# Kernel tuning notes

Measured on AMD Instinct MI355X. Metric: run time of the kernel, lower is better.

## Reference

```python
import jax, jax.numpy as jnp
import numpy as np

N, E = 50000, 800000
IN, HID, OUT = 256, 128, 128


def setup_inputs() -> dict:
    key = jax.random.key(0)
    ks = jax.random.split(key, 6)
    x = jax.random.normal(ks[0], (N, IN), dtype=jnp.float32)
    edge_index = jax.random.randint(ks[1], (2, E), 0, N, dtype=jnp.int32)
    # xavier_normal-ish scales (exact init values irrelevant for correctness baseline)
    W1 = jax.random.normal(ks[2], (IN, HID), dtype=jnp.float32) * (1.414 / np.sqrt(IN))
    att_src = jax.random.normal(ks[3], (HID,), dtype=jnp.float32) * 0.1
    att_dst = jax.random.normal(ks[4], (HID,), dtype=jnp.float32) * 0.1
    W2 = jax.random.normal(ks[5], (HID, OUT), dtype=jnp.float32) * (1.414 / np.sqrt(HID))
    return {"x": x, "edge_index": edge_index, "W1": W1,
            "att_src": att_src, "att_dst": att_dst, "W2": W2}


def _gat_layer(x, edge_index, W, a_src, a_dst):
    """GATConv(heads=1, concat=False, add_self_loops=False, dropout=0), attention=True."""
    n = x.shape[0]
    src, dst = edge_index[0], edge_index[1]  # message x_j = h[src], grouped by index = dst
    h = x @ W                                 # (N, C)
    e_src = h @ a_src                         # (N,) per-node attention logits
    e_dst = h @ a_dst                         # (N,)
    # per-edge: sigmoid(alpha_j + alpha_i), then scatter-softmax over dst neighborhoods
    alpha = jax.nn.sigmoid(e_src[src] + e_dst[dst])             # (E,)
    m = jax.ops.segment_max(alpha, dst, num_segments=n)          # stable softmax max
    ex = jnp.exp(alpha - m[dst])
    denom = jax.ops.segment_sum(ex, dst, num_segments=n)
    w = ex / denom[dst]                                          # (E,)
    # scatter-add aggregation of weighted source features; heads=1 so mean over heads is identity
    return jax.ops.segment_sum(h[src] * w[:, None], dst, num_segments=n)  # (N, C)


def reference(x, edge_index, W1, att_src, att_dst, W2):
    h1 = jax.nn.elu(_gat_layer(x, edge_index, W1, att_src, att_dst))
    # conv2 called with attention=False: mm(h1, W2).view(N,1,C).mean(1) == plain linear
    return h1 @ W2
```

## Files before the change

### kernel.cpp

```cpp
#include <hip/hip_runtime.h>
#include <hip/hip_bf16.h>

#define N_NODES 50000
#define N_EDGES 800000
#define DIN 256
#define DHID 128
#define DOUT 128
#define NBUCK 196
#define BINBLK 256
#define EPB 3125
#define G1TILES 391
#define HTP 136

typedef __attribute__((ext_vector_type(8))) short bf16x8;
typedef __attribute__((ext_vector_type(4))) float f32x4;

__device__ inline unsigned short f2b(float f) {
    __hip_bfloat16 b = __float2bfloat16(f);
    return *reinterpret_cast<unsigned short*>(&b);
}

__global__ __launch_bounds__(1024) void convW_lhist_kernel(
    const float* __restrict__ W1, const float* __restrict__ W2,
    const int* __restrict__ ei,
    unsigned short* __restrict__ W1t, unsigned short* __restrict__ W2t,
    int* __restrict__ blockHistT)
{
    __shared__ int h[NBUCK];
    const int blk = blockIdx.x;
    const int tid = threadIdx.x;

    if (blk < 48) {
        int i = blk * 1024 + tid;
        if (i < DIN * DHID) {
            int n = i >> 8, k = i & 255;
            int kt = k >> 5, q = (k >> 3) & 3, e = k & 7;
            int t = n >> 4, m = n & 15;
            W1t[(((kt * 8 + t) * 64) + (q * 16 + m)) * 8 + e] = f2b(W1[k * DHID + n]);
        } else {
            int j = i - DIN * DHID;
            int n = j >> 7, k = j & 127;
            int kt = k >> 5, q = (k >> 3) & 3, e = k & 7;
            int t = n >> 4, m = n & 15;
            W2t[(((kt * 8 + t) * 64) + (q * 16 + m)) * 8 + e] = f2b(W2[k * DOUT + n]);
        }
        return;
    }

    const int b = blk - 48;
    if (tid < NBUCK) h[tid] = 0;
    __syncthreads();
    const int base = b * EPB;
    #pragma unroll 1
    for (int it = 0; it < 4; ++it) {
        int e = base + it * 1024 + tid;
        if (e < base + EPB)
            atomicAdd(&h[ei[N_EDGES + e] >> 8], 1);
    }
    __syncthreads();
    if (tid < 256) blockHistT[b * 256 + tid] = (tid < NBUCK) ? h[tid] : 0;
}

__global__ __launch_bounds__(256) void gemm1_scan_kernel(
    const float* __restrict__ x,
    const unsigned short* __restrict__ W1t,
    const float* __restrict__ att_src,
    const float* __restrict__ att_dst,
    const int* __restrict__ blockHistT,
    unsigned short* __restrict__ hb,
    float* __restrict__ es,
    float* __restrict__ ed,
    int* __restrict__ matrixScan)
{
    __shared__ int bs[256];
    __shared__ int sc[256];
    const int tid = threadIdx.x;

    if (blockIdx.x >= G1TILES) {
        const int b = blockIdx.x - G1TILES;

        int tot = 0;
        #pragma unroll 4
        for (int p = 0; p < 256; ++p) tot += blockHistT[p * 256 + tid];
        bs[tid] = tot;
        __syncthreads();
        #pragma unroll
        for (int off = 1; off < 256; off <<= 1) {
            int u = (tid >= off) ? bs[tid - off] : 0;
            __syncthreads();
            bs[tid] += u;
            __syncthreads();
        }
        const int base = (b == 0) ? 0 : bs[b - 1];

        int c = blockHistT[tid * 256 + b];
        sc[tid] = c;
        __syncthreads();
        #pragma unroll
        for (int off = 1; off < 256; off <<= 1) {
            int u = (tid >= off) ? sc[tid - off] : 0;
            __syncthreads();
            sc[tid] += u;
            __syncthreads();
        }
        matrixScan[b * 256 + tid] = base + sc[tid] - c;
        return;
    }

    const int wave = tid >> 6, lane = tid & 63;
    const int row0 = blockIdx.x * 128 + wave * 32;
    const int m = lane & 15, q = lane >> 4;

    int r0 = row0 + m;
    int r1 = row0 + 16 + m;
    int rc0 = (r0 < N_NODES) ? r0 : 0;
    int rc1 = (r1 < N_NODES) ? r1 : 0;

    f32x4 acc0[8], acc1[8];
    #pragma unroll
    for (int t = 0; t < 8; ++t) {
        acc0[t] = (f32x4){0.f, 0.f, 0.f, 0.f};
        acc1[t] = (f32x4){0.f, 0.f, 0.f, 0.f};
    }

    const float* xr0 = x + (size_t)rc0 * DIN + q * 8;
    const float* xr1 = x + (size_t)rc1 * DIN + q * 8;
    const short* wb  = (const short*)W1t + lane * 8;

    #pragma unroll
    for (int kt = 0; kt < 8; ++kt) {
        float4 f0 = *(const float4*)(xr0 + kt * 32);
        float4 f1 = *(const float4*)(xr0 + kt * 32 + 4);
        float4 g0 = *(const float4*)(xr1 + kt * 32);
        float4 g1 = *(const float4*)(xr1 + kt * 32 + 4);
        bf16x8 a0, a1;
        a0[0] = (short)f2b(f0.x); a0[1] = (short)f2b(f0.y);
        a0[2] = (short)f2b(f0.z); a0[3] = (short)f2b(f0.w);
        a0[4] = (short)f2b(f1.x); a0[5] = (short)f2b(f1.y);
        a0[6] = (short)f2b(f1.z); a0[7] = (short)f2b(f1.w);
        a1[0] = (short)f2b(g0.x); a1[1] = (short)f2b(g0.y);
        a1[2] = (short)f2b(g0.z); a1[3] = (short)f2b(g0.w);
        a1[4] = (short)f2b(g1.x); a1[5] = (short)f2b(g1.y);
        a1[6] = (short)f2b(g1.z); a1[7] = (short)f2b(g1.w);
        #pragma unroll
        for (int t = 0; t < 8; ++t) {
            bf16x8 b = *(const bf16x8*)(wb + (kt * 8 + t) * 512);
            acc0[t] = __builtin_amdgcn_mfma_f32_16x16x32_bf16(a0, b, acc0[t], 0, 0, 0);
            acc1[t] = __builtin_amdgcn_mfma_f32_16x16x32_bf16(a1, b, acc1[t], 0, 0, 0);
        }
    }

    #pragma unroll
    for (int reg = 0; reg < 4; ++reg) {
        int ra = row0 + q * 4 + reg;
        int rb = row0 + 16 + q * 4 + reg;
        if (ra < N_NODES) {
            #pragma unroll
            for (int t = 0; t < 8; ++t)
                hb[(size_t)ra * DHID + t * 16 + m] = f2b(acc0[t][reg]);
        }
        if (rb < N_NODES) {
            #pragma unroll
            for (int t = 0; t < 8; ++t)
                hb[(size_t)rb * DHID + t * 16 + m] = f2b(acc1[t][reg]);
        }
    }

    float es0[4] = {0,0,0,0}, ed0[4] = {0,0,0,0};
    float es1[4] = {0,0,0,0}, ed1[4] = {0,0,0,0};
    #pragma unroll
    for (int t = 0; t < 8; ++t) {
        float as = att_src[t * 16 + m];
        float ad = att_dst[t * 16 + m];
        #pragma unroll
        for (int reg = 0; reg < 4; ++reg) {
            es0[reg] += acc0[t][reg] * as;
            ed0[reg] += acc0[t][reg] * ad;
            es1[reg] += acc1[t][reg] * as;
            ed1[reg] += acc1[t][reg] * ad;
        }
    }
    #pragma unroll
    for (int off = 8; off; off >>= 1)
        #pragma unroll
        for (int reg = 0; reg < 4; ++reg) {
            es0[reg] += __shfl_xor(es0[reg], off);
            ed0[reg] += __shfl_xor(ed0[reg], off);
            es1[reg] += __shfl_xor(es1[reg], off);
            ed1[reg] += __shfl_xor(ed1[reg], off);
        }
    if (m == 0) {
        #pragma unroll
        for (int reg = 0; reg < 4; ++reg) {
            int ra = row0 + q * 4 + reg;
            int rb = row0 + 16 + q * 4 + reg;
            if (ra < N_NODES) { es[ra] = es0[reg]; ed[ra] = ed0[reg]; }
            if (rb < N_NODES) { es[rb] = es1[reg]; ed[rb] = ed1[reg]; }
        }
    }
}

__global__ __launch_bounds__(1024) void binpass_kernel(
    const int* __restrict__ ei,
    const float* __restrict__ es,
    const float* __restrict__ ed,
    const int* __restrict__ matrixScan,
    int2* __restrict__ binned)
{
    __shared__ int lcur[NBUCK];
    const int t = threadIdx.x, blk = blockIdx.x;
    if (t < NBUCK) lcur[t] = matrixScan[t * 256 + blk];
    __syncthreads();
    const int base = blk * EPB;
    #pragma unroll 1
    for (int it = 0; it < 4; ++it) {
        int e = base + it * 1024 + t;
        if (e < base + EPB) {
            int s = ei[e];
            int d = ei[N_EDGES + e];
            float a  = es[s] + ed[d];
            float sg = 1.f / (1.f + __expf(-a));
            float w  = __expf(sg);
            int pos = atomicAdd(&lcur[d >> 8], 1);
            binned[pos] = make_int2(s | ((d & 255) << 16), __float_as_int(w));
        }
    }
}

__global__ __launch_bounds__(1024) void sortpass_kernel(
    const int2* __restrict__ binned,
    const int* __restrict__ matrixScan,
    int2* __restrict__ sortedSW,
    int* __restrict__ offset,
    int* __restrict__ count)
{
    __shared__ int lhist[256], lscan[256], lcur[256];
    const int t = threadIdx.x, b = blockIdx.x;
    const int start = matrixScan[b * 256];
    const int end   = (b == NBUCK - 1) ? N_EDGES : matrixScan[(b + 1) * 256];
    const int cnt   = end - start;

    if (t < 256) lhist[t] = 0;
    __syncthreads();
    for (int i = t; i < cnt; i += 1024)
        atomicAdd(&lhist[(binned[start + i].x >> 16) & 255], 1);
    __syncthreads();

    int v = 0;
    if (t < 256) { v = lhist[t]; lscan[t] = v; }
    __syncthreads();
    #pragma unroll
    for (int off = 1; off < 256; off <<= 1) {
        int u = 0;
        if (t < 256 && t >= off) u = lscan[t - off];
        __syncthreads();
        if (t < 256) lscan[t] += u;
        __syncthreads();
    }
    if (t < 256) {
        int excl = lscan[t] - v;
        int node = (b << 8) + t;
        if (node < N_NODES) { offset[node] = start + excl; count[node] = v; }
        lcur[t] = excl;
    }
    __syncthreads();

    for (int i = t; i < cnt; i += 1024) {
        int2 ent = binned[start + i];
        int dlow = (ent.x >> 16) & 255;
        int pos = atomicAdd(&lcur[dlow], 1);
        sortedSW[start + pos] = make_int2(ent.x & 0xFFFF, ent.y);
    }
}

__global__ __launch_bounds__(256) void aggemm2_kernel(
    const int2* __restrict__ sortedSW,
    const int* __restrict__ offset,
    const int* __restrict__ count,
    const unsigned short* __restrict__ hb,
    const unsigned short* __restrict__ W2t,
    float* __restrict__ out)
{
    __shared__ unsigned short ht[16][HTP];
    const int tid = threadIdx.x;
    const int wv = tid >> 6, lane = tid & 63;
    const int nbase = blockIdx.x * 16;

    #pragma unroll 1
    for (int s = 0; s < 4; ++s) {
        const int row = wv * 4 + s;
        const int node = nbase + row;

        int beg = offset[node];
        int deg = count[node];

        float2 acc = make_float2(0.f, 0.f);
        float wsum = 0.f;

        for (int bb = 0; bb < deg; bb += 64) {
            int cnt = min(64, deg - bb);
            int2 sw = (lane < cnt) ? sortedSW[beg + bb + lane] : make_int2(0, 0);
            int j = 0;

#define TIER(T)                                                                 \
            for (; j + T <= cnt; j += T) {                                      \
                unsigned uu[T]; float ww[T];                                    \
                _Pragma("unroll")                                               \
                for (int k = 0; k < T; ++k) {                                   \
                    int s_ = __builtin_amdgcn_readlane(sw.x, j + k);            \
                    uu[k] = *(const unsigned*)(hb + (size_t)s_ * DHID + 2 * lane);\
                }                                                               \
                _Pragma("unroll")                                               \
                for (int k = 0; k < T; ++k)                                     \
                    ww[k] = __uint_as_float(                                    \
                        (unsigned)__builtin_amdgcn_readlane(sw.y, j + k));      \
                _Pragma("unroll")                                               \
                for (int k = 0; k < T; ++k) {                                   \
                    wsum  += ww[k];                                             \
                    acc.x += ww[k] * __uint_as_float(uu[k] << 16);              \
                    acc.y += ww[k] * __uint_as_float(uu[k] & 0xffff0000u);      \
                }                                                               \
            }

            TIER(16)
            TIER(8)
            TIER(4)
#undef TIER
            for (; j < cnt; ++j) {
                int   sj = __builtin_amdgcn_readlane(sw.x, j);
                float wj = __uint_as_float((unsigned)__builtin_amdgcn_readlane(sw.y, j));
                unsigned u = *(const unsigned*)(hb + (size_t)sj * DHID + 2 * lane);
                acc.x += wj * __uint_as_float(u << 16);
                acc.y += wj * __uint_as_float(u & 0xffff0000u);
                wsum  += wj;
            }
        }
        float inv = (deg > 0) ? 1.f / wsum : 0.f;
        float v0 = acc.x * inv, v1 = acc.y * inv;
        float e0 = v0 > 0.f ? v0 : (__expf(v0) - 1.f);
        float e1 = v1 > 0.f ? v1 : (__expf(v1) - 1.f);
        *(unsigned*)&ht[row][2 * lane] =
            (unsigned)f2b(e0) | ((unsigned)f2b(e1) << 16);
    }
    __syncthreads();

    const int m = lane & 15, q = lane >> 4;

    f32x4 c0 = (f32x4){0.f, 0.f, 0.f, 0.f};
    f32x4 c1 = (f32x4){0.f, 0.f, 0.f, 0.f};

    const short* wb = (const short*)W2t + lane * 8;
    const int t0 = wv * 2, t1 = wv * 2 + 1;

    #pragma unroll
    for (int kt = 0; kt < 4; ++kt) {
        bf16x8 a = *(const bf16x8*)&ht[m][q * 8 + kt * 32];
        bf16x8 b0 = *(const bf16x8*)(wb + (kt * 8 + t0) * 512);
        bf16x8 b1 = *(const bf16x8*)(wb + (kt * 8 + t1) * 512);
        c0 = __builtin_amdgcn_mfma_f32_16x16x32_bf16(a, b0, c0, 0, 0, 0);
        c1 = __builtin_amdgcn_mfma_f32_16x16x32_bf16(a, b1, c1, 0, 0, 0);
    }

    #pragma unroll
    for (int reg = 0; reg < 4; ++reg) {
        int node = nbase + q * 4 + reg;
        out[(size_t)node * DOUT + t0 * 16 + m] = c0[reg];
        out[(size_t)node * DOUT + t1 * 16 + m] = c1[reg];
    }
}

extern "C" void kernel_launch(void* const* d_in, const int* in_sizes, int n_in,
                              void* d_out, int out_size, void* d_ws, size_t ws_size,
                              hipStream_t stream)
{
    const float* x    = (const float*)d_in[0];
    const int*   ei   = (const int*)d_in[1];
    const float* W1   = (const float*)d_in[2];
    const float* asrc = (const float*)d_in[3];
    const float* adst = (const float*)d_in[4];
    const float* W2   = (const float*)d_in[5];
    float*       out  = (float*)d_out;

    char* p = (char*)d_ws;
    unsigned short* hb  = (unsigned short*)p;  p += (size_t)N_NODES * DHID * 2;
    unsigned short* W1t = (unsigned short*)p;  p += (size_t)DHID * DIN * 2;
    unsigned short* W2t = (unsigned short*)p;  p += (size_t)DOUT * DHID * 2;
    float* es     = (float*)p;  p += (size_t)N_NODES * 4;
    float* ed     = (float*)p;  p += (size_t)N_NODES * 4;
    int*   offset = (int*)p;    p += (size_t)N_NODES * 4;
    int*   count  = (int*)p;    p += (size_t)N_NODES * 4;
    int*   blockHistT   = (int*)p; p += (size_t)256 * 256 * 4;
    int*   matrixScan   = (int*)p; p += (size_t)NBUCK * 256 * 4;
    int2*  binned   = (int2*)p; p += (size_t)N_EDGES * 8;
    int2*  sortedSW = (int2*)p; p += (size_t)N_EDGES * 8;

    convW_lhist_kernel<<<48 + BINBLK, 1024, 0, stream>>>(W1, W2, ei, W1t, W2t, blockHistT);

    gemm1_scan_kernel<<<G1TILES + NBUCK, 256, 0, stream>>>(
        x, W1t, asrc, adst, blockHistT, hb, es, ed, matrixScan);

    binpass_kernel<<<BINBLK, 1024, 0, stream>>>(ei, es, ed, matrixScan, binned);

    sortpass_kernel<<<NBUCK, 1024, 0, stream>>>(binned, matrixScan, sortedSW, offset, count);

    aggemm2_kernel<<<(N_NODES + 15) / 16, 256, 0, stream>>>(
        sortedSW, offset, count, hb, W2t, out);
}
```

Measured before the change: 183.9 us.

## Gather four edges per wave with 16-byte loads in aggregation kernel

```diff
diff --git a/kernel.cpp b/kernel.cpp
--- a/kernel.cpp
+++ b/kernel.cpp
@@ -286,6 +286,10 @@
     const int wv = tid >> 6, lane = tid & 63;
     const int nbase = blockIdx.x * 16;
 
+    const int  qlane = lane & 15;
+    const bool q1 = (lane >> 4) & 1;
+    const bool q2 = (lane >> 5) & 1;
+
     #pragma unroll 1
     for (int s = 0; s < 4; ++s) {
         const int row = wv * 4 + s;
@@ -294,7 +298,8 @@
         int beg = offset[node];
         int deg = count[node];
 
-        float2 acc = make_float2(0.f, 0.f);
+        float a0 = 0.f, a1 = 0.f, a2 = 0.f, a3 = 0.f;
+        float a4 = 0.f, a5 = 0.f, a6 = 0.f, a7 = 0.f;
         float wsum = 0.f;
 
         for (int bb = 0; bb < deg; bb += 64) {
@@ -302,45 +307,108 @@
             int2 sw = (lane < cnt) ? sortedSW[beg + bb + lane] : make_int2(0, 0);
             int j = 0;
 
-#define TIER(T)                                                                 \
-            for (; j + T <= cnt; j += T) {                                      \
-                unsigned uu[T]; float ww[T];                                    \
-                _Pragma("unroll")                                               \
-                for (int k = 0; k < T; ++k) {                                   \
-                    int s_ = __builtin_amdgcn_readlane(sw.x, j + k);            \
-                    uu[k] = *(const unsigned*)(hb + (size_t)s_ * DHID + 2 * lane);\
-                }                                                               \
-                _Pragma("unroll")                                               \
-                for (int k = 0; k < T; ++k)                                     \
-                    ww[k] = __uint_as_float(                                    \
-                        (unsigned)__builtin_amdgcn_readlane(sw.y, j + k));      \
-                _Pragma("unroll")                                               \
-                for (int k = 0; k < T; ++k) {                                   \
-                    wsum  += ww[k];                                             \
-                    acc.x += ww[k] * __uint_as_float(uu[k] << 16);              \
-                    acc.y += ww[k] * __uint_as_float(uu[k] & 0xffff0000u);      \
-                }                                                               \
+#define QTIER(T)                                                                 \
+            for (; j + 4 * T <= cnt; j += 4 * T) {                               \
+                uint4 uu[T]; float ww[T];                                        \
+                _Pragma("unroll")                                                \
+                for (int k = 0; k < T; ++k) {                                    \
+                    int s0 = __builtin_amdgcn_readlane(sw.x, j + 4 * k);         \
+                    int s1 = __builtin_amdgcn_readlane(sw.x, j + 4 * k + 1);     \
+                    int s2 = __builtin_amdgcn_readlane(sw.x, j + 4 * k + 2);     \
+                    int s3 = __builtin_amdgcn_readlane(sw.x, j + 4 * k + 3);     \
+                    int sl = q1 ? s1 : s0;                                       \
+                    int sh = q1 ? s3 : s2;                                       \
+                    int ss = q2 ? sh : sl;                                       \
+                    uu[k] = *(const uint4*)(hb + (size_t)ss * DHID + 8 * qlane); \
+                }                                                                \
+                _Pragma("unroll")                                                \
+                for (int k = 0; k < T; ++k) {                                    \
+                    unsigned w0 = (unsigned)__builtin_amdgcn_readlane(sw.y, j + 4 * k);     \
+                    unsigned w1 = (unsigned)__builtin_amdgcn_readlane(sw.y, j + 4 * k + 1); \
+                    unsigned w2 = (unsigned)__builtin_amdgcn_readlane(sw.y, j + 4 * k + 2); \
+                    unsigned w3 = (unsigned)__builtin_amdgcn_readlane(sw.y, j + 4 * k + 3); \
+                    unsigned wl = q1 ? w1 : w0;                                  \
+                    unsigned wh = q1 ? w3 : w2;                                  \
+                    ww[k] = __uint_as_float(q2 ? wh : wl);                       \
+                }                                                                \
+                _Pragma("unroll")                                                \
+                for (int k = 0; k < T; ++k) {                                    \
+                    float w = ww[k];                                             \
+                    wsum += w;                                                   \
+                    a0 += w * __uint_as_float(uu[k].x << 16);                    \
+                    a1 += w * __uint_as_float(uu[k].x & 0xffff0000u);            \
+                    a2 += w * __uint_as_float(uu[k].y << 16);                    \
+                    a3 += w * __uint_as_float(uu[k].y & 0xffff0000u);            \
+                    a4 += w * __uint_as_float(uu[k].z << 16);                    \
+                    a5 += w * __uint_as_float(uu[k].z & 0xffff0000u);            \
+                    a6 += w * __uint_as_float(uu[k].w << 16);                    \
+                    a7 += w * __uint_as_float(uu[k].w & 0xffff0000u);            \
+                }                                                                \
             }
 
-            TIER(16)
-            TIER(8)
-            TIER(4)
-#undef TIER
-            for (; j < cnt; ++j) {
-                int   sj = __builtin_amdgcn_readlane(sw.x, j);
-                float wj = __uint_as_float((unsigned)__builtin_amdgcn_readlane(sw.y, j));
-                unsigned u = *(const unsigned*)(hb + (size_t)sj * DHID + 2 * lane);
-                acc.x += wj * __uint_as_float(u << 16);
-                acc.y += wj * __uint_as_float(u & 0xffff0000u);
-                wsum  += wj;
+            QTIER(8)
+            QTIER(4)
+            QTIER(2)
+            QTIER(1)
+#undef QTIER
+            if (j < cnt) {
+                int last = cnt - 1;
+                int r = cnt - j;
+                int s0 = __builtin_amdgcn_readlane(sw.x, j);
+                int s1 = __builtin_amdgcn_readlane(sw.x, min(j + 1, last));
+                int s2 = __builtin_amdgcn_readlane(sw.x, min(j + 2, last));
+                int sl = q1 ? s1 : s0;
+                int sh = q1 ? s2 : s2;
+                int ss = q2 ? sh : sl;
+                uint4 u = *(const uint4*)(hb + (size_t)ss * DHID + 8 * qlane);
+                unsigned w0 = (unsigned)__builtin_amdgcn_readlane(sw.y, j);
+                unsigned w1 = (unsigned)__builtin_amdgcn_readlane(sw.y, min(j + 1, last));
+                unsigned w2 = (unsigned)__builtin_amdgcn_readlane(sw.y, min(j + 2, last));
+                int qq = (lane >> 4);
+                unsigned wl = q1 ? w1 : w0;
+                unsigned wh = w2;
+                float w = (qq < r) ? __uint_as_float(q2 ? wh : wl) : 0.f;
+                wsum += w;
+                a0 += w * __uint_as_float(u.x << 16);
+                a1 += w * __uint_as_float(u.x & 0xffff0000u);
+                a2 += w * __uint_as_float(u.y << 16);
+                a3 += w * __uint_as_float(u.y & 0xffff0000u);
+                a4 += w * __uint_as_float(u.z << 16);
+                a5 += w * __uint_as_float(u.z & 0xffff0000u);
+                a6 += w * __uint_as_float(u.w << 16);
+                a7 += w * __uint_as_float(u.w & 0xffff0000u);
             }
         }
+
+        a0 += __shfl_xor(a0, 16); a0 += __shfl_xor(a0, 32);
+        a1 += __shfl_xor(a1, 16); a1 += __shfl_xor(a1, 32);
+        a2 += __shfl_xor(a2, 16); a2 += __shfl_xor(a2, 32);
+        a3 += __shfl_xor(a3, 16); a3 += __shfl_xor(a3, 32);
+        a4 += __shfl_xor(a4, 16); a4 += __shfl_xor(a4, 32);
+        a5 += __shfl_xor(a5, 16); a5 += __shfl_xor(a5, 32);
+        a6 += __shfl_xor(a6, 16); a6 += __shfl_xor(a6, 32);
+        a7 += __shfl_xor(a7, 16); a7 += __shfl_xor(a7, 32);
+        wsum += __shfl_xor(wsum, 16); wsum += __shfl_xor(wsum, 32);
+
         float inv = (deg > 0) ? 1.f / wsum : 0.f;
-        float v0 = acc.x * inv, v1 = acc.y * inv;
+        float v0 = a0 * inv, v1 = a1 * inv, v2 = a2 * inv, v3 = a3 * inv;
+        float v4 = a4 * inv, v5 = a5 * inv, v6 = a6 * inv, v7 = a7 * inv;
         float e0 = v0 > 0.f ? v0 : (__expf(v0) - 1.f);
         float e1 = v1 > 0.f ? v1 : (__expf(v1) - 1.f);
-        *(unsigned*)&ht[row][2 * lane] =
-            (unsigned)f2b(e0) | ((unsigned)f2b(e1) << 16);
+        float e2 = v2 > 0.f ? v2 : (__expf(v2) - 1.f);
+        float e3 = v3 > 0.f ? v3 : (__expf(v3) - 1.f);
+        float e4 = v4 > 0.f ? v4 : (__expf(v4) - 1.f);
+        float e5 = v5 > 0.f ? v5 : (__expf(v5) - 1.f);
+        float e6 = v6 > 0.f ? v6 : (__expf(v6) - 1.f);
+        float e7 = v7 > 0.f ? v7 : (__expf(v7) - 1.f);
+        if (lane < 16) {
+            uint4 pk;
+            pk.x = (unsigned)f2b(e0) | ((unsigned)f2b(e1) << 16);
+            pk.y = (unsigned)f2b(e2) | ((unsigned)f2b(e3) << 16);
+            pk.z = (unsigned)f2b(e4) | ((unsigned)f2b(e5) << 16);
+            pk.w = (unsigned)f2b(e6) | ((unsigned)f2b(e7) << 16);
+            *(uint4*)&ht[row][8 * lane] = pk;
+        }
     }
     __syncthreads();
 
```

Result: slower. 190.6 us (+3.7%).

## Fuse per-bucket sort with aggregation and second GEMM using shared-memory edge buffer

Applied to the files above, without the earlier changes.

```diff
diff --git a/kernel.cpp b/kernel.cpp
--- a/kernel.cpp
+++ b/kernel.cpp
@@ -11,6 +11,7 @@
 #define EPB 3125
 #define G1TILES 391
 #define HTP 136
+#define EBCAP 8192
 
 typedef __attribute__((ext_vector_type(8))) short bf16x8;
 typedef __attribute__((ext_vector_type(4))) float f32x4;
@@ -227,145 +228,142 @@
     }
 }
 
-__global__ __launch_bounds__(1024) void sortpass_kernel(
+__global__ __launch_bounds__(1024) void sortaggemm_kernel(
     const int2* __restrict__ binned,
     const int* __restrict__ matrixScan,
-    int2* __restrict__ sortedSW,
-    int* __restrict__ offset,
-    int* __restrict__ count)
-{
-    __shared__ int lhist[256], lscan[256], lcur[256];
-    const int t = threadIdx.x, b = blockIdx.x;
-    const int start = matrixScan[b * 256];
-    const int end   = (b == NBUCK - 1) ? N_EDGES : matrixScan[(b + 1) * 256];
-    const int cnt   = end - start;
-
-    if (t < 256) lhist[t] = 0;
-    __syncthreads();
-    for (int i = t; i < cnt; i += 1024)
-        atomicAdd(&lhist[(binned[start + i].x >> 16) & 255], 1);
-    __syncthreads();
-
-    int v = 0;
-    if (t < 256) { v = lhist[t]; lscan[t] = v; }
-    __syncthreads();
-    #pragma unroll
-    for (int off = 1; off < 256; off <<= 1) {
-        int u = 0;
-        if (t < 256 && t >= off) u = lscan[t - off];
-        __syncthreads();
-        if (t < 256) lscan[t] += u;
-        __syncthreads();
-    }
-    if (t < 256) {
-        int excl = lscan[t] - v;
-        int node = (b << 8) + t;
-        if (node < N_NODES) { offset[node] = start + excl; count[node] = v; }
-        lcur[t] = excl;
-    }
-    __syncthreads();
-
-    for (int i = t; i < cnt; i += 1024) {
-        int2 ent = binned[start + i];
-        int dlow = (ent.x >> 16) & 255;
-        int pos = atomicAdd(&lcur[dlow], 1);
-        sortedSW[start + pos] = make_int2(ent.x & 0xFFFF, ent.y);
-    }
-}
-
-__global__ __launch_bounds__(256) void aggemm2_kernel(
-    const int2* __restrict__ sortedSW,
-    const int* __restrict__ offset,
-    const int* __restrict__ count,
     const unsigned short* __restrict__ hb,
     const unsigned short* __restrict__ W2t,
     float* __restrict__ out)
 {
-    __shared__ unsigned short ht[16][HTP];
+    __shared__ int2 eb[EBCAP];
+    __shared__ int lhist[256], lscan[256], lcur[256];
+    __shared__ unsigned short ht[64][HTP];
     const int tid = threadIdx.x;
+    const int b = blockIdx.x;
     const int wv = tid >> 6, lane = tid & 63;
-    const int nbase = blockIdx.x * 16;
+
+    const int start = matrixScan[b * 256];
+    const int end   = (b == NBUCK - 1) ? N_EDGES : matrixScan[(b + 1) * 256];
+    const int cnt   = end - start;
+
+    if (tid < 256) lhist[tid] = 0;
+    __syncthreads();
+    for (int i = tid; i < cnt; i += 1024)
+        atomicAdd(&lhist[(binned[start + i].x >> 16) & 255], 1);
+    __syncthreads();
+
+    int v = 0;
+    if (tid < 256) { v = lhist[tid]; lscan[tid] = v; }
+    __syncthreads();
+    #pragma unroll
+    for (int off = 1; off < 256; off <<= 1) {
+        int u = 0;
+        if (tid < 256 && tid >= off) u = lscan[tid - off];
+        __syncthreads();
+        if (tid < 256) lscan[tid] += u;
+        __syncthreads();
+    }
+    if (tid < 256) lcur[tid] = lscan[tid] - v;
+    __syncthreads();
+
+    for (int i = tid; i < cnt; i += 1024) {
+        int2 ent = binned[start + i];
+        int dlow = (ent.x >> 16) & 255;
+        int pos = atomicAdd(&lcur[dlow], 1);
+        eb[pos] = make_int2(ent.x & 0xFFFF, ent.y);
+    }
+    __syncthreads();
 
     #pragma unroll 1
-    for (int s = 0; s < 4; ++s) {
-        const int row = wv * 4 + s;
-        const int node = nbase + row;
-
-        int beg = offset[node];
-        int deg = count[node];
-
-        float2 acc = make_float2(0.f, 0.f);
-        float wsum = 0.f;
-
-        for (int bb = 0; bb < deg; bb += 64) {
-            int cnt = min(64, deg - bb);
-            int2 sw = (lane < cnt) ? sortedSW[beg + bb + lane] : make_int2(0, 0);
-            int j = 0;
+    for (int r4 = 0; r4 < 4; ++r4) {
+        const int base64 = r4 * 64;
+
+        #pragma unroll 1
+        for (int s = 0; s < 4; ++s) {
+            const int row = wv * 4 + s;
+            const int dlow = base64 + row;
+            const int beg = lscan[dlow] - lhist[dlow];
+            const int deg = lhist[dlow];
+
+            float2 acc = make_float2(0.f, 0.f);
+            float wsum = 0.f;
+
+            for (int bb = 0; bb < deg; bb += 64) {
+                int c_ = min(64, deg - bb);
+                int2 sw = (lane < c_) ? eb[beg + bb + lane] : make_int2(0, 0);
+                int j = 0;
 
 #define TIER(T)                                                                 \
-            for (; j + T <= cnt; j += T) {                                      \
-                unsigned uu[T]; float ww[T];                                    \
-                _Pragma("unroll")                                               \
-                for (int k = 0; k < T; ++k) {                                   \
-                    int s_ = __builtin_amdgcn_readlane(sw.x, j + k);            \
-                    uu[k] = *(const unsigned*)(hb + (size_t)s_ * DHID + 2 * lane);\
-                }                                                               \
-                _Pragma("unroll")                                               \
-                for (int k = 0; k < T; ++k)                                     \
-                    ww[k] = __uint_as_float(                                    \
-                        (unsigned)__builtin_amdgcn_readlane(sw.y, j + k));      \
-                _Pragma("unroll")                                               \
-                for (int k = 0; k < T; ++k) {                                   \
-                    wsum  += ww[k];                                             \
-                    acc.x += ww[k] * __uint_as_float(uu[k] << 16);              \
-                    acc.y += ww[k] * __uint_as_float(uu[k] & 0xffff0000u);      \
-                }                                                               \
+                for (; j + T <= c_; j += T) {                                   \
+                    unsigned uu[T]; float ww[T];                                \
+                    _Pragma("unroll")                                           \
+                    for (int k = 0; k < T; ++k) {                               \
+                        int s_ = __builtin_amdgcn_readlane(sw.x, j + k);        \
+                        uu[k] = *(const unsigned*)(hb + (size_t)s_ * DHID + 2 * lane); \
+                    }                                                           \
+                    _Pragma("unroll")                                           \
+                    for (int k = 0; k < T; ++k)                                 \
+                        ww[k] = __uint_as_float(                                \
+                            (unsigned)__builtin_amdgcn_readlane(sw.y, j + k));  \
+                    _Pragma("unroll")                                           \
+                    for (int k = 0; k < T; ++k) {                               \
+                        wsum  += ww[k];                                         \
+                        acc.x += ww[k] * __uint_as_float(uu[k] << 16);          \
+                        acc.y += ww[k] * __uint_as_float(uu[k] & 0xffff0000u);  \
+                    }                                                           \
+                }
+
+                TIER(16)
+                TIER(8)
+                TIER(4)
+#undef TIER
+                for (; j < c_; ++j) {
+                    int   sj = __builtin_amdgcn_readlane(sw.x, j);
+                    float wj = __uint_as_float((unsigned)__builtin_amdgcn_readlane(sw.y, j));
+                    unsigned u = *(const unsigned*)(hb + (size_t)sj * DHID + 2 * lane);
+                    acc.x += wj * __uint_as_float(u << 16);
+                    acc.y += wj * __uint_as_float(u & 0xffff0000u);
+                    wsum  += wj;
+                }
             }
-
-            TIER(16)
-            TIER(8)
-            TIER(4)
-#undef TIER
-            for (; j < cnt; ++j) {
-                int   sj = __builtin_amdgcn_readlane(sw.x, j);
-                float wj = __uint_as_float((unsigned)__builtin_amdgcn_readlane(sw.y, j));
-                unsigned u = *(const unsigned*)(hb + (size_t)sj * DHID + 2 * lane);
-                acc.x += wj * __uint_as_float(u << 16);
-                acc.y += wj * __uint_as_float(u & 0xffff0000u);
-                wsum  += wj;
+            float inv = (deg > 0) ? 1.f / wsum : 0.f;
+            float v0 = acc.x * inv, v1 = acc.y * inv;
+            float e0 = v0 > 0.f ? v0 : (__expf(v0) - 1.f);
+            float e1 = v1 > 0.f ? v1 : (__expf(v1) - 1.f);
+            *(unsigned*)&ht[row][2 * lane] =
+                (unsigned)f2b(e0) | ((unsigned)f2b(e1) << 16);
+        }
+        __syncthreads();
+
+        {
+            const int m = lane & 15, q = lane >> 4;
+            const int rg = wv & 3;
+            const int t0 = (wv >> 2) * 2, t1 = t0 + 1;
+            const int arow = rg * 16 + m;
+
+            f32x4 c0 = (f32x4){0.f, 0.f, 0.f, 0.f};
+            f32x4 c1 = (f32x4){0.f, 0.f, 0.f, 0.f};
+            const short* wb = (const short*)W2t + lane * 8;
+
+            #pragma unroll
+            for (int kt = 0; kt < 4; ++kt) {
+                bf16x8 a = *(const bf16x8*)&ht[arow][q * 8 + kt * 32];
+                bf16x8 b0 = *(const bf16x8*)(wb + (kt * 8 + t0) * 512);
+                bf16x8 b1 = *(const bf16x8*)(wb + (kt * 8 + t1) * 512);
+                c0 = __builtin_amdgcn_mfma_f32_16x16x32_bf16(a, b0, c0, 0, 0, 0);
+                c1 = __builtin_amdgcn_mfma_f32_16x16x32_bf16(a, b1, c1, 0, 0, 0);
             }
-        }
-        float inv = (deg > 0) ? 1.f / wsum : 0.f;
-        float v0 = acc.x * inv, v1 = acc.y * inv;
-        float e0 = v0 > 0.f ? v0 : (__expf(v0) - 1.f);
-        float e1 = v1 > 0.f ? v1 : (__expf(v1) - 1.f);
-        *(unsigned*)&ht[row][2 * lane] =
-            (unsigned)f2b(e0) | ((unsigned)f2b(e1) << 16);
-    }
-    __syncthreads();
-
-    const int m = lane & 15, q = lane >> 4;
-
-    f32x4 c0 = (f32x4){0.f, 0.f, 0.f, 0.f};
-    f32x4 c1 = (f32x4){0.f, 0.f, 0.f, 0.f};
-
-    const short* wb = (const short*)W2t + lane * 8;
-    const int t0 = wv * 2, t1 = wv * 2 + 1;
-
-    #pragma unroll
-    for (int kt = 0; kt < 4; ++kt) {
-        bf16x8 a = *(const bf16x8*)&ht[m][q * 8 + kt * 32];
-        bf16x8 b0 = *(const bf16x8*)(wb + (kt * 8 + t0) * 512);
-        bf16x8 b1 = *(const bf16x8*)(wb + (kt * 8 + t1) * 512);
-        c0 = __builtin_amdgcn_mfma_f32_16x16x32_bf16(a, b0, c0, 0, 0, 0);
-        c1 = __builtin_amdgcn_mfma_f32_16x16x32_bf16(a, b1, c1, 0, 0, 0);
-    }
-
-    #pragma unroll
-    for (int reg = 0; reg < 4; ++reg) {
-        int node = nbase + q * 4 + reg;
-        out[(size_t)node * DOUT + t0 * 16 + m] = c0[reg];
-        out[(size_t)node * DOUT + t1 * 16 + m] = c1[reg];
+
+            #pragma unroll
+            for (int reg = 0; reg < 4; ++reg) {
+                int node = (b << 8) + base64 + rg * 16 + q * 4 + reg;
+                if (node < N_NODES) {
+                    out[(size_t)node * DOUT + t0 * 16 + m] = c0[reg];
+                    out[(size_t)node * DOUT + t1 * 16 + m] = c1[reg];
+                }
+            }
+        }
+        __syncthreads();
     }
 }
 
@@ -387,12 +385,9 @@
     unsigned short* W2t = (unsigned short*)p;  p += (size_t)DOUT * DHID * 2;
     float* es     = (float*)p;  p += (size_t)N_NODES * 4;
     float* ed     = (float*)p;  p += (size_t)N_NODES * 4;
-    int*   offset = (int*)p;    p += (size_t)N_NODES * 4;
-    int*   count  = (int*)p;    p += (size_t)N_NODES * 4;
     int*   blockHistT   = (int*)p; p += (size_t)256 * 256 * 4;
     int*   matrixScan   = (int*)p; p += (size_t)NBUCK * 256 * 4;
     int2*  binned   = (int2*)p; p += (size_t)N_EDGES * 8;
-    int2*  sortedSW = (int2*)p; p += (size_t)N_EDGES * 8;
 
     convW_lhist_kernel<<<48 + BINBLK, 1024, 0, stream>>>(W1, W2, ei, W1t, W2t, blockHistT);
 
@@ -401,8 +396,6 @@
 
     binpass_kernel<<<BINBLK, 1024, 0, stream>>>(ei, es, ed, matrixScan, binned);
 
-    sortpass_kernel<<<NBUCK, 1024, 0, stream>>>(binned, matrixScan, sortedSW, offset, count);
-
-    aggemm2_kernel<<<(N_NODES + 15) / 16, 256, 0, stream>>>(
-        sortedSW, offset, count, hb, W2t, out);
-}
+    sortaggemm_kernel<<<NBUCK, 1024, 0, stream>>>(
+        binned, matrixScan, hb, W2t, out);
+}
```

Result: no change. 185.9 us (+1.1%).
